# Performance work log

Hardware: AMD Instinct MI355X
Metric: run time of the kernel (lower is better)

The kernel has to match this reference:

```python
import jax, jax.numpy as jnp
import numpy as np

T, KBLK, EMB, B = 2048, 64, 512, 4


def _make_coords(t, k):
    # head1: for each j, cols = block_start(j) + arange(j % k + 1)  (block-causal local)
    j = np.arange(t)
    cnt1 = (j % k) + 1
    rows1 = np.repeat(j, cnt1)
    off1 = np.arange(cnt1.sum()) - np.repeat(np.cumsum(cnt1) - cnt1, cnt1)
    cols1 = (rows1 // k) * k + off1
    # head2: for each block start c, rows = arange(c, t), col = c  (strided block-start)
    starts = np.arange(t // k) * k
    cnt2 = t - starts
    base = np.repeat(starts, cnt2)
    off2 = np.arange(cnt2.sum()) - np.repeat(np.cumsum(cnt2) - cnt2, cnt2)
    rows2, cols2 = base + off2, base
    c1 = np.stack([rows1, cols1], 1).astype(np.int32)
    c2 = np.stack([rows2, cols2], 1).astype(np.int32)
    return c1, c2


def setup_inputs() -> dict:
    key = jax.random.key(0)
    ks = jax.random.split(key, 6)
    s = 1.0 / float(np.sqrt(EMB))
    c1, c2 = _make_coords(T, KBLK)
    return {
        "x": jax.random.normal(ks[0], (B, T, EMB), jnp.float32),
        "Wk": jax.random.normal(ks[1], (EMB, EMB), jnp.float32) * s,
        "bk": jnp.zeros((EMB,), jnp.float32),
        "Wq": jax.random.normal(ks[2], (EMB, EMB), jnp.float32) * s,
        "bq": jnp.zeros((EMB,), jnp.float32),
        "Wv": jax.random.normal(ks[3], (EMB, EMB), jnp.float32) * s,
        "bv": jnp.zeros((EMB,), jnp.float32),
        "Wu": jax.random.normal(ks[4], (EMB, 2 * EMB), jnp.float32) * s,
        "bu": jnp.zeros((EMB,), jnp.float32),
        "coords1": jnp.asarray(c1),
        "coords2": jnp.asarray(c2),
    }


def _sparse_head(Kt, Qt, Vt, coords):
    rows, cols = coords[:, 0], coords[:, 1]
    # dot[b,p] = (K @ Q^T)[b, rows[p], cols[p]] = K[b,rows[p],:] . Q[b,cols[p],:]
    dot = jnp.einsum('bpe,bpe->bp', Kt[:, rows], Qt[:, cols])
    # sparse.batchmm: out[b,r] = sum_{p: rows[p]=r} dot[b,p] * V[b, cols[p]]
    out = jnp.zeros_like(Vt).at[:, rows].add(dot[..., None] * Vt[:, cols])
    return out


def reference(x, Wk, bk, Wq, bq, Wv, bv, Wu, bu, coords1, coords2):
    Kt = x @ Wk.T + bk
    Qt = x @ Wq.T + bq
    Vt = x @ Wv.T + bv
    h1 = _sparse_head(Kt, Qt, Vt, coords1)
    h2 = _sparse_head(Kt, Qt, Vt, coords2)
    comb = jnp.concatenate([h1, h2], axis=-1)  # [B, T, 2*EMB]
    return comb @ Wu.T + bu
```

## Files before the change

kernel.cpp:

```cpp
#include <hip/hip_runtime.h>


typedef unsigned short u16;
typedef __attribute__((ext_vector_type(8))) short short8;
typedef __attribute__((ext_vector_type(4))) float f32x4;

constexpr int TDIM  = 2048;
constexpr int EMB_D = 512;
constexpr int BB    = 4;
constexpr int NBLK  = 32;
constexpr int LDK   = 2048;

__device__ __forceinline__ u16 f2b(float f) {
    unsigned u = __float_as_uint(f);
    unsigned r = (u + 0x7FFFu + ((u >> 16) & 1u)) >> 16;
    return (u16)r;
}

__global__ __launch_bounds__(256) void prep_k(
    const float* __restrict__ x, const float* __restrict__ Wk, const float* __restrict__ Wq,
    const float* __restrict__ Wv, const float* __restrict__ Wu,
    const float* __restrict__ bk, const float* __restrict__ bq, const float* __restrict__ bv,
    u16* __restrict__ xb, u16* __restrict__ wcat, float* __restrict__ biascat)
{
    const int bid = blockIdx.x, tid = threadIdx.x;
    if (bid < 4608) {
        const float* src; u16* dst; int base;
        if (bid < 4096)      { src = x;  dst = xb;            base = bid * 1024; }
        else if (bid < 4352) { src = Wk; dst = wcat;          base = (bid - 4096) * 1024; }
        else                 { src = Wq; dst = wcat + 262144; base = (bid - 4352) * 1024; }
        const int idx = base + tid * 4;
        float4 v = *(const float4*)(src + idx);
        ushort4 o = { f2b(v.x), f2b(v.y), f2b(v.z), f2b(v.w) };
        *(ushort4*)(dst + idx) = o;
    } else if (bid < 4864) {
        const int local = bid - 4608;
        const int half = local >> 7, rem = local & 127;
        const int n0 = (rem >> 3) * 32, k0 = (rem & 7) * 64;
        __shared__ float Wus[32][33];
        __shared__ float Wvs[32][68];
        const int n = tid >> 3, kc = (tid & 7) * 8;
        float acc[8] = {};
        for (int j0 = 0; j0 < 512; j0 += 32) {
            __syncthreads();
            {
                const int r = tid >> 3, c4 = (tid & 7) * 4;
                float4 a = *(const float4*)(Wu + (size_t)(n0 + r) * 1024 + half * 512 + j0 + c4);
                Wus[r][c4+0]=a.x; Wus[r][c4+1]=a.y; Wus[r][c4+2]=a.z; Wus[r][c4+3]=a.w;
            }
            {
                const int r = tid >> 3, c8 = (tid & 7) * 8;
                float4 a  = *(const float4*)(Wv + (size_t)(j0 + r) * 512 + k0 + c8);
                float4 a2 = *(const float4*)(Wv + (size_t)(j0 + r) * 512 + k0 + c8 + 4);
                *(float4*)(&Wvs[r][c8])     = a;
                *(float4*)(&Wvs[r][c8 + 4]) = a2;
            }
            __syncthreads();
            #pragma unroll
            for (int j = 0; j < 32; ++j) {
                const float a = Wus[n][j];
                float4 v0 = *(const float4*)(&Wvs[j][kc]);
                float4 v1 = *(const float4*)(&Wvs[j][kc + 4]);
                acc[0]+=a*v0.x; acc[1]+=a*v0.y; acc[2]+=a*v0.z; acc[3]+=a*v0.w;
                acc[4]+=a*v1.x; acc[5]+=a*v1.y; acc[6]+=a*v1.z; acc[7]+=a*v1.w;
            }
        }
        #pragma unroll
        for (int l = 0; l < 8; ++l)
            wcat[(size_t)(1024 + half * 512 + n0 + n) * 512 + k0 + kc + l] = f2b(acc[l]);
    } else {
        const int g = (bid - 4864) * 256 + tid;
        if (g < 512) biascat[g] = bk[g];
        else if (g < 1024) biascat[g] = bq[g - 512];
        else {
            const int n = (g - 1024) & 511, half = (g - 1024) >> 9;
            float s = 0.f;
            const float* wr = Wu + (size_t)n * 1024 + half * 512;
            for (int j = 0; j < 512; j += 4) {
                float4 a = *(const float4*)(wr + j);
                float4 b = *(const float4*)(bv + j);
                s += a.x*b.x + a.y*b.y + a.z*b.z + a.w*b.w;
            }
            biascat[g] = s;
        }
    }
}

__global__ __launch_bounds__(256) void kqv_gemm_k(
    const u16* __restrict__ A, const u16* __restrict__ W,
    const float* __restrict__ bias, u16* __restrict__ C)
{
    __shared__ u16 As[128 * 32];
    __shared__ u16 Bs[128 * 32];
    const int bm = blockIdx.x * 128;
    const int bn = blockIdx.y * 128;
    const int tid  = threadIdx.x;
    const int wid  = tid >> 6;
    const int lane = tid & 63;
    const int l15  = lane & 15;
    const int quad = lane >> 4;
    const int wm = (wid & 1) * 64;
    const int wn = (wid >> 1) * 64;

    f32x4 acc[4][4] = {};

    const int srow  = tid >> 2;
    const int skoff = (tid & 3) * 8;
    const u16* Ag = A + (size_t)(bm + srow) * EMB_D + skoff;
    const u16* Wg = W + (size_t)(bn + srow) * EMB_D + skoff;
    char* AsBase = (char*)As + wid * 1024;
    char* BsBase = (char*)Bs + wid * 1024;

    for (int k0 = 0; k0 < EMB_D; k0 += 32) {
        __syncthreads();
        __builtin_amdgcn_global_load_lds(
            (const __attribute__((address_space(1))) void*)(Ag + k0),
            (__attribute__((address_space(3))) void*)AsBase, 16, 0, 0);
        __builtin_amdgcn_global_load_lds(
            (const __attribute__((address_space(1))) void*)(Ag + (size_t)64 * EMB_D + k0),
            (__attribute__((address_space(3))) void*)(AsBase + 4096), 16, 0, 0);
        __builtin_amdgcn_global_load_lds(
            (const __attribute__((address_space(1))) void*)(Wg + k0),
            (__attribute__((address_space(3))) void*)BsBase, 16, 0, 0);
        __builtin_amdgcn_global_load_lds(
            (const __attribute__((address_space(1))) void*)(Wg + (size_t)64 * EMB_D + k0),
            (__attribute__((address_space(3))) void*)(BsBase + 4096), 16, 0, 0);
        __syncthreads();

        short8 a[4], b[4];
        #pragma unroll
        for (int i = 0; i < 4; ++i)
            a[i] = *(const short8*)((const short*)As + (wm + 16 * i + l15) * 32 + quad * 8);
        #pragma unroll
        for (int j = 0; j < 4; ++j)
            b[j] = *(const short8*)((const short*)Bs + (wn + 16 * j + l15) * 32 + quad * 8);
        #pragma unroll
        for (int i = 0; i < 4; ++i)
            #pragma unroll
            for (int j = 0; j < 4; ++j)
                acc[i][j] = __builtin_amdgcn_mfma_f32_16x16x32_bf16(a[i], b[j], acc[i][j], 0, 0, 0);
    }

    #pragma unroll
    for (int i = 0; i < 4; ++i) {
        #pragma unroll
        for (int j = 0; j < 4; ++j) {
            const int col = bn + wn + 16 * j + l15;
            const float bvv = bias[col];
            #pragma unroll
            for (int r = 0; r < 4; ++r) {
                const int row = bm + wm + 16 * i + quad * 4 + r;
                C[(size_t)row * LDK + col] = f2b(acc[i][j][r] + bvv);
            }
        }
    }
}

__global__ __launch_bounds__(256) void heads_k(
    const u16* __restrict__ KQV, const float* __restrict__ bu, float* __restrict__ out)
{
    __shared__ u16 smA[64 * 104];
    __shared__ u16 smVT[128 * 104];
    __shared__ u16 pK[2][64 * 32];
    __shared__ u16 pQ[2][64 * 32];
    __shared__ u16 pQs[2][32 * 32];

    const int blk = blockIdx.x, b = blockIdx.y;
    const int e0 = blockIdx.z * 128;
    const int tid = threadIdx.x;
    const int wid = tid >> 6, lane = tid & 63;
    const int l15 = lane & 15, quad = lane >> 4;
    const size_t row0 = (size_t)b * TDIM + (size_t)blk * 64;
    const size_t brow = (size_t)b * TDIM;
    const int srow_base = 16 * wid + quad * 4;

    #pragma unroll
    for (int it = 0; it < 4; ++it) {
        const int id = tid + 256 * it;
        const int c  = id & 63;
        const int eo = (id >> 6) * 8;
        short8 v = *(const short8*)(KQV + (row0 + c) * (size_t)LDK + 1024 + e0 + eo);
        #pragma unroll
        for (int i = 0; i < 8; ++i) smVT[(eo + i) * 104 + c] = (u16)v[i];
    }
    #pragma unroll
    for (int it = 0; it < 2; ++it) {
        const int id = tid + 256 * it;
        const int m  = id & 31;
        const int eo = (id >> 5) * 8;
        short8 v = *(const short8*)(KQV + (brow + 64 * m) * (size_t)LDK + 1536 + e0 + eo);
        #pragma unroll
        for (int i = 0; i < 8; ++i) smVT[(eo + i) * 104 + 64 + m] = (u16)v[i];
    }

    f32x4 s1[4] = {}; f32x4 s2[2] = {};
    const int srow  = tid >> 2;
    const int skoff = (tid & 3) * 8;
    const int qsrow = srow & 31;
    const int qsp   = tid >> 7;
    const u16* Kg  = KQV + (row0 + srow) * (size_t)LDK + skoff;
    const u16* Qg  = KQV + (row0 + srow) * (size_t)LDK + 512 + skoff;
    const u16* Qsg = KQV + (brow + (size_t)64 * qsrow) * (size_t)LDK + 512 + qsp * 32 + skoff;
    char* dK  = (char*)pK  + wid * 1024;
    char* dQ  = (char*)pQ  + wid * 1024;
    char* dQs = (char*)pQs + wid * 1024;

    for (int k0 = 0; k0 < 512; k0 += 64) {
        __syncthreads();
        __builtin_amdgcn_global_load_lds(
            (const __attribute__((address_space(1))) void*)(Kg + k0),
            (__attribute__((address_space(3))) void*)dK, 16, 0, 0);
        __builtin_amdgcn_global_load_lds(
            (const __attribute__((address_space(1))) void*)(Kg + k0 + 32),
            (__attribute__((address_space(3))) void*)(dK + 4096), 16, 0, 0);
        __builtin_amdgcn_global_load_lds(
            (const __attribute__((address_space(1))) void*)(Qg + k0),
            (__attribute__((address_space(3))) void*)dQ, 16, 0, 0);
        __builtin_amdgcn_global_load_lds(
            (const __attribute__((address_space(1))) void*)(Qg + k0 + 32),
            (__attribute__((address_space(3))) void*)(dQ + 4096), 16, 0, 0);
        __builtin_amdgcn_global_load_lds(
            (const __attribute__((address_space(1))) void*)(Qsg + k0),
            (__attribute__((address_space(3))) void*)dQs, 16, 0, 0);
        __syncthreads();

        short8 a0 = *(const short8*)(pK[0] + (16 * wid + l15) * 32 + quad * 8);
        short8 a1 = *(const short8*)(pK[1] + (16 * wid + l15) * 32 + quad * 8);
        #pragma unroll
        for (int j = 0; j < 4; ++j) {
            short8 b0 = *(const short8*)(pQ[0] + (16 * j + l15) * 32 + quad * 8);
            short8 b1 = *(const short8*)(pQ[1] + (16 * j + l15) * 32 + quad * 8);
            s1[j] = __builtin_amdgcn_mfma_f32_16x16x32_bf16(a0, b0, s1[j], 0, 0, 0);
            s1[j] = __builtin_amdgcn_mfma_f32_16x16x32_bf16(a1, b1, s1[j], 0, 0, 0);
        }
        #pragma unroll
        for (int j = 0; j < 2; ++j) {
            short8 b0 = *(const short8*)(pQs[0] + (16 * j + l15) * 32 + quad * 8);
            short8 b1 = *(const short8*)(pQs[1] + (16 * j + l15) * 32 + quad * 8);
            s2[j] = __builtin_amdgcn_mfma_f32_16x16x32_bf16(a0, b0, s2[j], 0, 0, 0);
            s2[j] = __builtin_amdgcn_mfma_f32_16x16x32_bf16(a1, b1, s2[j], 0, 0, 0);
        }
    }

    #pragma unroll
    for (int j = 0; j < 4; ++j)
        #pragma unroll
        for (int r = 0; r < 4; ++r) {
            const int rr = srow_base + r;
            const int cc = 16 * j + l15;
            smA[rr * 104 + cc] = f2b((cc <= rr) ? s1[j][r] : 0.0f);
        }
    #pragma unroll
    for (int j = 0; j < 2; ++j)
        #pragma unroll
        for (int r = 0; r < 4; ++r) {
            const int m  = 16 * j + l15;
            const int rr = srow_base + r;
            smA[rr * 104 + 64 + m] = f2b((m <= blk) ? s2[j][r] : 0.0f);
        }
    __syncthreads();

    f32x4 o[8] = {};
    const u16* arow = smA + (16 * wid + l15) * 104;
    #pragma unroll
    for (int ks = 0; ks < 3; ++ks) {
        short8 as = *(const short8*)(arow + 32 * ks + quad * 8);
        #pragma unroll
        for (int nt = 0; nt < 8; ++nt) {
            short8 bs = *(const short8*)(smVT + (16 * nt + l15) * 104 + 32 * ks + quad * 8);
            o[nt] = __builtin_amdgcn_mfma_f32_16x16x32_bf16(as, bs, o[nt], 0, 0, 0);
        }
    }
    #pragma unroll
    for (int nt = 0; nt < 8; ++nt) {
        const int col = e0 + 16 * nt + l15;
        const float bvv = bu[col];
        #pragma unroll
        for (int r = 0; r < 4; ++r)
            out[(row0 + srow_base + r) * (size_t)EMB_D + col] = o[nt][r] + bvv;
    }
}

extern "C" void kernel_launch(void* const* d_in, const int* in_sizes, int n_in,
                              void* d_out, int out_size, void* d_ws, size_t ws_size,
                              hipStream_t stream)
{
    const float* x  = (const float*)d_in[0];
    const float* Wk = (const float*)d_in[1];
    const float* bk = (const float*)d_in[2];
    const float* Wq = (const float*)d_in[3];
    const float* bq = (const float*)d_in[4];
    const float* Wv = (const float*)d_in[5];
    const float* bv = (const float*)d_in[6];
    const float* Wu = (const float*)d_in[7];
    const float* bu = (const float*)d_in[8];
    float* out = (float*)d_out;

    char* w = (char*)d_ws;
    u16*   KQV     = (u16*)  (w + ((size_t)0  << 20));
    u16*   xb      = (u16*)  (w + ((size_t)32 << 20));
    u16*   wcat    = (u16*)  (w + ((size_t)40 << 20));
    float* biascat = (float*)(w + ((size_t)44 << 20));

    dim3 blk(256);
    hipLaunchKernelGGL(prep_k, dim3(4872), blk, 0, stream,
                       x, Wk, Wq, Wv, Wu, bk, bq, bv, xb, wcat, biascat);
    hipLaunchKernelGGL(kqv_gemm_k, dim3(64, 16), blk, 0, stream, xb, wcat, biascat, KQV);
    hipLaunchKernelGGL(heads_k, dim3(NBLK, BB, 4), blk, 0, stream, KQV, bu, out);
}
```

Before: 169.3 us.

## Compute fused Wu·Wv weight product with bf16 MFMA GEMM instead of scalar FMA

```diff
diff --git a/kernel.cpp b/kernel.cpp
--- a/kernel.cpp
+++ b/kernel.cpp
@@ -21,74 +21,64 @@
     const float* __restrict__ x, const float* __restrict__ Wk, const float* __restrict__ Wq,
     const float* __restrict__ Wv, const float* __restrict__ Wu,
     const float* __restrict__ bk, const float* __restrict__ bq, const float* __restrict__ bv,
-    u16* __restrict__ xb, u16* __restrict__ wcat, float* __restrict__ biascat)
+    u16* __restrict__ xb, u16* __restrict__ wcat, u16* __restrict__ wvtb,
+    u16* __restrict__ wub, float* __restrict__ biascat)
 {
     const int bid = blockIdx.x, tid = threadIdx.x;
-    if (bid < 4608) {
+    if (bid < 5120) {
         const float* src; u16* dst; int base;
         if (bid < 4096)      { src = x;  dst = xb;            base = bid * 1024; }
         else if (bid < 4352) { src = Wk; dst = wcat;          base = (bid - 4096) * 1024; }
-        else                 { src = Wq; dst = wcat + 262144; base = (bid - 4352) * 1024; }
+        else if (bid < 4608) { src = Wq; dst = wcat + 262144; base = (bid - 4352) * 1024; }
+        else                 { src = Wu; dst = wub;           base = (bid - 4608) * 1024; }
         const int idx = base + tid * 4;
         float4 v = *(const float4*)(src + idx);
         ushort4 o = { f2b(v.x), f2b(v.y), f2b(v.z), f2b(v.w) };
         *(ushort4*)(dst + idx) = o;
-    } else if (bid < 4864) {
-        const int local = bid - 4608;
-        const int half = local >> 7, rem = local & 127;
-        const int n0 = (rem >> 3) * 32, k0 = (rem & 7) * 64;
-        __shared__ float Wus[32][33];
-        __shared__ float Wvs[32][68];
-        const int n = tid >> 3, kc = (tid & 7) * 8;
-        float acc[8] = {};
-        for (int j0 = 0; j0 < 512; j0 += 32) {
-            __syncthreads();
-            {
-                const int r = tid >> 3, c4 = (tid & 7) * 4;
-                float4 a = *(const float4*)(Wu + (size_t)(n0 + r) * 1024 + half * 512 + j0 + c4);
-                Wus[r][c4+0]=a.x; Wus[r][c4+1]=a.y; Wus[r][c4+2]=a.z; Wus[r][c4+3]=a.w;
-            }
-            {
-                const int r = tid >> 3, c8 = (tid & 7) * 8;
-                float4 a  = *(const float4*)(Wv + (size_t)(j0 + r) * 512 + k0 + c8);
-                float4 a2 = *(const float4*)(Wv + (size_t)(j0 + r) * 512 + k0 + c8 + 4);
-                *(float4*)(&Wvs[r][c8])     = a;
-                *(float4*)(&Wvs[r][c8 + 4]) = a2;
-            }
-            __syncthreads();
-            #pragma unroll
-            for (int j = 0; j < 32; ++j) {
-                const float a = Wus[n][j];
-                float4 v0 = *(const float4*)(&Wvs[j][kc]);
-                float4 v1 = *(const float4*)(&Wvs[j][kc + 4]);
-                acc[0]+=a*v0.x; acc[1]+=a*v0.y; acc[2]+=a*v0.z; acc[3]+=a*v0.w;
-                acc[4]+=a*v1.x; acc[5]+=a*v1.y; acc[6]+=a*v1.z; acc[7]+=a*v1.w;
-            }
-        }
-        #pragma unroll
-        for (int l = 0; l < 8; ++l)
-            wcat[(size_t)(1024 + half * 512 + n0 + n) * 512 + k0 + kc + l] = f2b(acc[l]);
+    } else if (bid < 5184) {
+        __shared__ float T[64][65];
+        const int t = bid - 5120;
+        const int j0 = (t >> 3) * 64, k0 = (t & 7) * 64;
+        const int rr = tid >> 4, c4 = (tid & 15) * 4;
+        #pragma unroll
+        for (int it = 0; it < 4; ++it) {
+            const int j = rr + it * 16;
+            float4 v = *(const float4*)(Wv + (size_t)(j0 + j) * 512 + k0 + c4);
+            T[c4+0][j] = v.x; T[c4+1][j] = v.y; T[c4+2][j] = v.z; T[c4+3][j] = v.w;
+        }
+        __syncthreads();
+        #pragma unroll
+        for (int it = 0; it < 4; ++it) {
+            const int k = rr + it * 16;
+            ushort4 o = { f2b(T[k][c4+0]), f2b(T[k][c4+1]), f2b(T[k][c4+2]), f2b(T[k][c4+3]) };
+            *(ushort4*)(wvtb + (size_t)(k0 + k) * 512 + j0 + c4) = o;
+        }
+    } else if (bid < 5200) {
+        const int o = (bid - 5184) * 64 + (tid >> 2);
+        const int p = tid & 3;
+        const int n = o & 511, half = o >> 9;
+        const float* wr = Wu + (size_t)n * 1024 + half * 512 + p * 128;
+        const float* br = bv + p * 128;
+        float s = 0.f;
+        #pragma unroll
+        for (int j = 0; j < 128; j += 4) {
+            float4 a = *(const float4*)(wr + j);
+            float4 b = *(const float4*)(br + j);
+            s += a.x*b.x + a.y*b.y + a.z*b.z + a.w*b.w;
+        }
+        s += __shfl_xor(s, 1);
+        s += __shfl_xor(s, 2);
+        if (p == 0) biascat[1024 + o] = s;
     } else {
-        const int g = (bid - 4864) * 256 + tid;
-        if (g < 512) biascat[g] = bk[g];
-        else if (g < 1024) biascat[g] = bq[g - 512];
-        else {
-            const int n = (g - 1024) & 511, half = (g - 1024) >> 9;
-            float s = 0.f;
-            const float* wr = Wu + (size_t)n * 1024 + half * 512;
-            for (int j = 0; j < 512; j += 4) {
-                float4 a = *(const float4*)(wr + j);
-                float4 b = *(const float4*)(bv + j);
-                s += a.x*b.x + a.y*b.y + a.z*b.z + a.w*b.w;
-            }
-            biascat[g] = s;
-        }
-    }
-}
-
-__global__ __launch_bounds__(256) void kqv_gemm_k(
-    const u16* __restrict__ A, const u16* __restrict__ W,
-    const float* __restrict__ bias, u16* __restrict__ C)
+        const int idx = tid * 4;
+        float4 v = (idx < 512) ? *(const float4*)(bk + idx)
+                               : *(const float4*)(bq + idx - 512);
+        *(float4*)(biascat + idx) = v;
+    }
+}
+
+__global__ __launch_bounds__(256) void wc_gemm_k(
+    const u16* __restrict__ wub, const u16* __restrict__ wvtb, u16* __restrict__ wcat)
 {
     __shared__ u16 As[128 * 32];
     __shared__ u16 Bs[128 * 32];
@@ -106,6 +96,76 @@
 
     const int srow  = tid >> 2;
     const int skoff = (tid & 3) * 8;
+    const int m0 = bm + srow, m1 = bm + 64 + srow;
+    const u16* Ag0 = wub + (size_t)(m0 & 511) * 1024 + (m0 >> 9) * 512 + skoff;
+    const u16* Ag1 = wub + (size_t)(m1 & 511) * 1024 + (m1 >> 9) * 512 + skoff;
+    const u16* Bg  = wvtb + (size_t)(bn + srow) * 512 + skoff;
+    char* AsBase = (char*)As + wid * 1024;
+    char* BsBase = (char*)Bs + wid * 1024;
+
+    for (int k0 = 0; k0 < 512; k0 += 32) {
+        __syncthreads();
+        __builtin_amdgcn_global_load_lds(
+            (const __attribute__((address_space(1))) void*)(Ag0 + k0),
+            (__attribute__((address_space(3))) void*)AsBase, 16, 0, 0);
+        __builtin_amdgcn_global_load_lds(
+            (const __attribute__((address_space(1))) void*)(Ag1 + k0),
+            (__attribute__((address_space(3))) void*)(AsBase + 4096), 16, 0, 0);
+        __builtin_amdgcn_global_load_lds(
+            (const __attribute__((address_space(1))) void*)(Bg + k0),
+            (__attribute__((address_space(3))) void*)BsBase, 16, 0, 0);
+        __builtin_amdgcn_global_load_lds(
+            (const __attribute__((address_space(1))) void*)(Bg + (size_t)64 * 512 + k0),
+            (__attribute__((address_space(3))) void*)(BsBase + 4096), 16, 0, 0);
+        __syncthreads();
+
+        short8 a[4], b[4];
+        #pragma unroll
+        for (int i = 0; i < 4; ++i)
+            a[i] = *(const short8*)((const short*)As + (wm + 16 * i + l15) * 32 + quad * 8);
+        #pragma unroll
+        for (int j = 0; j < 4; ++j)
+            b[j] = *(const short8*)((const short*)Bs + (wn + 16 * j + l15) * 32 + quad * 8);
+        #pragma unroll
+        for (int i = 0; i < 4; ++i)
+            #pragma unroll
+            for (int j = 0; j < 4; ++j)
+                acc[i][j] = __builtin_amdgcn_mfma_f32_16x16x32_bf16(a[i], b[j], acc[i][j], 0, 0, 0);
+    }
+
+    #pragma unroll
+    for (int i = 0; i < 4; ++i)
+        #pragma unroll
+        for (int j = 0; j < 4; ++j) {
+            const int col = bn + wn + 16 * j + l15;
+            #pragma unroll
+            for (int r = 0; r < 4; ++r) {
+                const int row = bm + wm + 16 * i + quad * 4 + r;
+                wcat[(size_t)(1024 + row) * 512 + col] = f2b(acc[i][j][r]);
+            }
+        }
+}
+
+__global__ __launch_bounds__(256) void kqv_gemm_k(
+    const u16* __restrict__ A, const u16* __restrict__ W,
+    const float* __restrict__ bias, u16* __restrict__ C)
+{
+    __shared__ u16 As[128 * 32];
+    __shared__ u16 Bs[128 * 32];
+    const int bm = blockIdx.x * 128;
+    const int bn = blockIdx.y * 128;
+    const int tid  = threadIdx.x;
+    const int wid  = tid >> 6;
+    const int lane = tid & 63;
+    const int l15  = lane & 15;
+    const int quad = lane >> 4;
+    const int wm = (wid & 1) * 64;
+    const int wn = (wid >> 1) * 64;
+
+    f32x4 acc[4][4] = {};
+
+    const int srow  = tid >> 2;
+    const int skoff = (tid & 3) * 8;
     const u16* Ag = A + (size_t)(bm + srow) * EMB_D + skoff;
     const u16* Wg = W + (size_t)(bn + srow) * EMB_D + skoff;
     char* AsBase = (char*)As + wid * 1024;
@@ -300,11 +360,14 @@
     u16*   KQV     = (u16*)  (w + ((size_t)0  << 20));
     u16*   xb      = (u16*)  (w + ((size_t)32 << 20));
     u16*   wcat    = (u16*)  (w + ((size_t)40 << 20));
+    u16*   wvtb    = (u16*)  (w + ((size_t)42 << 20));
+    u16*   wub     = (u16*)  (w + ((size_t)43 << 20));
     float* biascat = (float*)(w + ((size_t)44 << 20));
 
     dim3 blk(256);
-    hipLaunchKernelGGL(prep_k, dim3(4872), blk, 0, stream,
-                       x, Wk, Wq, Wv, Wu, bk, bq, bv, xb, wcat, biascat);
+    hipLaunchKernelGGL(prep_k, dim3(5201), blk, 0, stream,
+                       x, Wk, Wq, Wv, Wu, bk, bq, bv, xb, wcat, wvtb, wub, biascat);
+    hipLaunchKernelGGL(wc_gemm_k, dim3(8, 4), blk, 0, stream, wub, wvtb, wcat);
     hipLaunchKernelGGL(kqv_gemm_k, dim3(64, 16), blk, 0, stream, xb, wcat, biascat, KQV);
     hipLaunchKernelGGL(heads_k, dim3(NBLK, BB, 4), blk, 0, stream, KQV, bu, out);
 }
```

After: 147.6 us. 1.15x faster.
